# Performance work log

Measured on AMD Instinct MI355X. Metric: run time of the kernel, lower is better.

Reference implementation:

```python
import jax, jax.numpy as jnp
import numpy as np

H = 32          # hidden_size
NUM_LAYERS = 3
B, T, IN = 16384, 64, 2


def _gru_dir(x, Wih, Whh, bih, bhh, reverse):
    """Single-direction GRU over x:[B,T,I] with PyTorch gate math."""
    # Precompute input projections for all timesteps: [B,T,3H]
    xg = jnp.einsum('bti,gi->btg', x, Wih) + bih
    if reverse:
        xg = xg[:, ::-1]

    def step(h, xt):
        gh = h @ Whh.T + bhh                      # [B,3H]
        xr, xz, xn = jnp.split(xt, 3, axis=-1)
        hr, hz, hn = jnp.split(gh, 3, axis=-1)
        r = jax.nn.sigmoid(xr + hr)
        z = jax.nn.sigmoid(xz + hz)
        n = jnp.tanh(xn + r * hn)
        h2 = (1.0 - z) * n + z * h
        return h2, h2

    h0 = jnp.zeros((x.shape[0], H), x.dtype)
    _, hs = jax.lax.scan(step, h0, jnp.swapaxes(xg, 0, 1))  # [T,B,H]
    hs = jnp.swapaxes(hs, 0, 1)                              # [B,T,H]
    if reverse:
        hs = hs[:, ::-1]
    return hs


def setup_inputs() -> dict:
    key = jax.random.key(0)
    ks = jax.random.split(key, 11)
    s = 0.2  # weight scale ~ uniform(-1/sqrt(H)) magnitude
    return {
        'x':    jax.random.normal(ks[0], (B, T, IN), jnp.float32),
        'Wih0': jax.random.normal(ks[1], (2, 3 * H, IN), jnp.float32) * s,
        'Whh0': jax.random.normal(ks[2], (2, 3 * H, H), jnp.float32) * s,
        'bih0': jax.random.normal(ks[3], (2, 3 * H), jnp.float32) * s,
        'bhh0': jax.random.normal(ks[4], (2, 3 * H), jnp.float32) * s,
        'Wih':  jax.random.normal(ks[5], (NUM_LAYERS - 1, 2, 3 * H, 2 * H), jnp.float32) * s,
        'Whh':  jax.random.normal(ks[6], (NUM_LAYERS - 1, 2, 3 * H, H), jnp.float32) * s,
        'bih':  jax.random.normal(ks[7], (NUM_LAYERS - 1, 2, 3 * H), jnp.float32) * s,
        'bhh':  jax.random.normal(ks[8], (NUM_LAYERS - 1, 2, 3 * H), jnp.float32) * s,
        'Wfc':  jax.random.normal(ks[9], (2, 2 * H), jnp.float32) * s,
        'bfc':  jax.random.normal(ks[10], (2,), jnp.float32) * s,
    }


def reference(x, Wih0, Whh0, bih0, bhh0, Wih, Whh, bih, bhh, Wfc, bfc):
    out = x
    for l in range(NUM_LAYERS):
        if l == 0:
            wi, wh, bi, bh = Wih0, Whh0, bih0, bhh0
        else:
            wi, wh, bi, bh = Wih[l - 1], Whh[l - 1], bih[l - 1], bhh[l - 1]
        fwd = _gru_dir(out, wi[0], wh[0], bi[0], bh[0], reverse=False)
        bwd = _gru_dir(out, wi[1], wh[1], bi[1], bh[1], reverse=True)
        out = jnp.concatenate([fwd, bwd], axis=-1)  # [B,T,2H]
    y = out @ Wfc.T + bfc                            # [B,T,2]
    return jnp.tanh(y)
```

## Files before the change

kernel.cpp:

```cpp
#include <hip/hip_runtime.h>
#include <cstdint>
#include <cstddef>


#define BB 16384
#define TT 64
#define PS ((size_t)BB * 32)
#define DS ((size_t)TT * PS)
#define PT ((size_t)TT * BB * 2)

typedef __attribute__((ext_vector_type(8))) _Float16 f16x8;
typedef __attribute__((ext_vector_type(4))) float f32x4;
typedef __attribute__((ext_vector_type(2))) float f32x2;

#if __has_builtin(__builtin_amdgcn_exp2f)
#define EXP2(x) __builtin_amdgcn_exp2f(x)
#else
#define EXP2(x) exp2f(x)
#endif
#if __has_builtin(__builtin_amdgcn_rcpf)
#define RCP(x) __builtin_amdgcn_rcpf(x)
#else
#define RCP(x) (1.0f / (x))
#endif

#define SR (-1.4426950408889634f)
#define SN (-2.8853900817779268f)

__device__ __forceinline__ f32x2 mk2(float a, float b) {
    f32x2 v; v.x = a; v.y = b; return v;
}
__device__ __forceinline__ float tanh_fast(float x) { return 2.0f / (1.0f + __expf(-2.0f * x)) - 1.0f; }
__device__ __forceinline__ unsigned short f2h(float f) {
    _Float16 h = (_Float16)f;
    return __builtin_bit_cast(unsigned short, h);
}
__device__ __forceinline__ unsigned int cvt_pkh(float a, float b) {
#if __has_builtin(__builtin_amdgcn_cvt_pkrtz)
    typedef __fp16 h2_t __attribute__((ext_vector_type(2)));
    h2_t p = __builtin_amdgcn_cvt_pkrtz(a, b);
    return __builtin_bit_cast(unsigned int, p);
#else
    return (unsigned int)f2h(a) | ((unsigned int)f2h(b) << 16);
#endif
}
__device__ __forceinline__ f32x4 mfma16h(f16x8 a, f16x8 b, f32x4 c) {
    return __builtin_amdgcn_mfma_f32_16x16x32_f16(a, b, c, 0, 0, 0);
}

__device__ __forceinline__ void gate_pair2(f32x2 aR, f32x2 aZ, f32x2 xN, f32x2 hN,
                                           f32x2& hp) {
    f32x2 er = mk2(EXP2(aR.x), EXP2(aR.y));
    f32x2 ez = mk2(EXP2(aZ.x), EXP2(aZ.y));
    f32x2 Ar = er + 1.f;
    f32x2 Az = ez + 1.f;
    float iR = RCP(Ar.x * Ar.y);
    float iZ = RCP(Az.x * Az.y);
    f32x2 r = mk2(iR * Ar.y, iR * Ar.x);
    f32x2 z = mk2(iZ * Az.y, iZ * Az.x);
    f32x2 v = r * hN + xN;
    f32x2 en = mk2(EXP2(v.x), EXP2(v.y));
    f32x2 An = en + 1.f;
    float iN = RCP(An.x * An.y);
    f32x2 n = mk2(fmaf(2.f, iN * An.y, -1.f), fmaf(2.f, iN * An.x, -1.f));
    hp = z * (hp - n) + n;
}


template<bool IS_L0, bool IS_LAST>
__global__ __launch_bounds__(256, 2)
void gru_mfma(const float* __restrict__ x0,
              const unsigned short* __restrict__ bin,
              const float* __restrict__ Wih,
              const float* __restrict__ Whh,
              const float* __restrict__ bih,
              const float* __restrict__ bhh,
              unsigned short* __restrict__ bout,
              const float* __restrict__ Wfc,
              float* __restrict__ pbase)
{
    const int tid  = threadIdx.x;
    const int lane = tid & 63;
    const int wv   = tid >> 6;
    const int g    = blockIdx.x * 4 + wv;
    const int d    = g >> 10;
    const int b0   = (g & 1023) * 16;
    const int col  = lane & 15;
    const int qd   = lane >> 4;

    f16x8 whhF[6];
    {
        const float* wsrc = Whh + d * 96 * 32;
        #pragma unroll
        for (int t = 0; t < 6; ++t) {
            const float sc = (t < 4) ? SR : SN;
            const int row = (t >> 1) * 32 + 8 * (col >> 2) + 4 * (t & 1) + (col & 3);
            const float* pr = wsrc + row * 32 + qd * 8;
            unsigned short wbits[8];
            #pragma unroll
            for (int j = 0; j < 8; ++j) wbits[j] = f2h(pr[j] * sc);
            whhF[t] = __builtin_bit_cast(f16x8, *(uint4*)wbits);
        }
    }

    f16x8 wihF[6][2];
    float w0c[6][4], w1c[6][4];
    if constexpr (!IS_L0) {
        const float* wsrc = Wih + d * 96 * 64;
        #pragma unroll
        for (int t = 0; t < 6; ++t) {
            const float sc = (t < 4) ? SR : SN;
            const int row = (t >> 1) * 32 + 8 * (col >> 2) + 4 * (t & 1) + (col & 3);
            #pragma unroll
            for (int kc = 0; kc < 2; ++kc) {
                const float* pr = wsrc + row * 64 + kc * 32 + qd * 8;
                unsigned short wbits[8];
                #pragma unroll
                for (int j = 0; j < 8; ++j) wbits[j] = f2h(pr[j] * sc);
                wihF[t][kc] = __builtin_bit_cast(f16x8, *(uint4*)wbits);
            }
        }
    } else {
        #pragma unroll
        for (int t = 0; t < 6; ++t) {
            const float sc = (t < 4) ? SR : SN;
            #pragma unroll
            for (int q = 0; q < 4; ++q) {
                const int row = (t >> 1) * 32 + 8 * qd + 4 * (t & 1) + q;
                const float* pr = Wih + d * 96 * 2 + row * 2;
                w0c[t][q] = pr[0] * sc;
                w1c[t][q] = pr[1] * sc;
            }
        }
    }

    f32x4 biasIn[6], biasHN[2];
    {
        const float* bi = bih + d * 96;
        const float* bh = bhh + d * 96;
        #pragma unroll
        for (int t = 0; t < 4; ++t) {
            const int off = (t >> 1) * 32 + 8 * qd + 4 * (t & 1);
            float4 a = *(const float4*)(bi + off);
            float4 b = *(const float4*)(bh + off);
            biasIn[t][0] = (a.x + b.x) * SR; biasIn[t][1] = (a.y + b.y) * SR;
            biasIn[t][2] = (a.z + b.z) * SR; biasIn[t][3] = (a.w + b.w) * SR;
        }
        #pragma unroll
        for (int T = 0; T < 2; ++T) {
            const int off = 64 + 8 * qd + 4 * T;
            float4 a = *(const float4*)(bi + off);
            float4 b = *(const float4*)(bh + off);
            biasIn[4 + T][0] = a.x * SN; biasIn[4 + T][1] = a.y * SN;
            biasIn[4 + T][2] = a.z * SN; biasIn[4 + T][3] = a.w * SN;
            biasHN[T][0] = b.x * SN; biasHN[T][1] = b.y * SN;
            biasHN[T][2] = b.z * SN; biasHN[T][3] = b.w * SN;
        }
    }

    float wf0[2][4], wf1[2][4];
    if constexpr (IS_LAST) {
        #pragma unroll
        for (int T = 0; T < 2; ++T)
            #pragma unroll
            for (int q = 0; q < 4; ++q) {
                const int u = 8 * qd + 4 * T + q;
                wf0[T][q] = Wfc[d * 32 + u];
                wf1[T][q] = Wfc[64 + d * 32 + u];
            }
    }

    const int t0 = d ? (TT - 1) : 0;
    const int dt = d ? -1 : 1;
    const ptrdiff_t dplane = (ptrdiff_t)dt * (ptrdiff_t)PS;

    f16x8 hF = {};
    float hprev[2][4] = {{0.f,0.f,0.f,0.f},{0.f,0.f,0.f,0.f}};

    auto REC = [&](f32x4 (&acc)[6], f32x4 (&accHN)[2]) {
        #pragma unroll
        for (int t = 0; t < 4; ++t)
            acc[t] = mfma16h(whhF[t], hF, acc[t]);
        #pragma unroll
        for (int T = 0; T < 2; ++T)
            accHN[T] = mfma16h(whhF[4 + T], hF, biasHN[T]);
    };

    auto PROJ = [&](f32x4 (&accN)[6], uint4 nx0, uint4 nx1, float2 nxs) {
        if constexpr (!IS_L0) {
            f16x8 a0 = __builtin_bit_cast(f16x8, nx0);
            f16x8 a1 = __builtin_bit_cast(f16x8, nx1);
            #pragma unroll
            for (int t = 0; t < 6; ++t) {
                accN[t] = mfma16h(wihF[t][0], a0, biasIn[t]);
                accN[t] = mfma16h(wihF[t][1], a1, accN[t]);
            }
        } else {
            #pragma unroll
            for (int t = 0; t < 6; ++t)
                #pragma unroll
                for (int q = 0; q < 4; ++q)
                    accN[t][q] = fmaf(nxs.x, w0c[t][q], fmaf(nxs.y, w1c[t][q], biasIn[t][q]));
        }
    };

    auto GATES = [&](f32x4 (&acc)[6], f32x4 (&accHN)[2], unsigned short* outp,
                     uint4& hwP, unsigned short*& opP, float* poutp) {
        unsigned int hw[4];
        #pragma unroll
        for (int T = 0; T < 2; ++T) {
            f32x2 hp01 = mk2(hprev[T][0], hprev[T][1]);
            f32x2 hp23 = mk2(hprev[T][2], hprev[T][3]);
            gate_pair2(mk2(acc[T][0], acc[T][1]), mk2(acc[2 + T][0], acc[2 + T][1]),
                       mk2(acc[4 + T][0], acc[4 + T][1]), mk2(accHN[T][0], accHN[T][1]), hp01);
            gate_pair2(mk2(acc[T][2], acc[T][3]), mk2(acc[2 + T][2], acc[2 + T][3]),
                       mk2(acc[4 + T][2], acc[4 + T][3]), mk2(accHN[T][2], accHN[T][3]), hp23);
            hprev[T][0] = hp01.x; hprev[T][1] = hp01.y;
            hprev[T][2] = hp23.x; hprev[T][3] = hp23.y;
            hw[2 * T]     = cvt_pkh(hp01.x, hp01.y);
            hw[2 * T + 1] = cvt_pkh(hp23.x, hp23.y);
        }
        hF = __builtin_bit_cast(f16x8, *(uint4*)hw);
        if constexpr (IS_LAST) {
            float p0 = 0.f, p1 = 0.f;
            #pragma unroll
            for (int T = 0; T < 2; ++T)
                #pragma unroll
                for (int q = 0; q < 4; ++q) {
                    p0 = fmaf(hprev[T][q], wf0[T][q], p0);
                    p1 = fmaf(hprev[T][q], wf1[T][q], p1);
                }
            p0 += __shfl_xor(p0, 16); p0 += __shfl_xor(p0, 32);
            p1 += __shfl_xor(p1, 16); p1 += __shfl_xor(p1, 32);
            if (qd == 0) *(float2*)poutp = make_float2(p0, p1);
        } else {
            *(uint4*)opP = hwP;
            hwP = *(uint4*)hw;
            opP = outp;
        }
    };

    f32x4 accA[6], accB[6], accHN[2];
    uint4 xc0 = {}, xc1 = {}, xe0 = {}, xe1 = {};
    float2 xsc = {}, xse = {};
    const unsigned short* xFE = nullptr; const unsigned short* xBE = nullptr;
    const unsigned short* xFO = nullptr; const unsigned short* xBO = nullptr;
    const float* xfpE = nullptr; const float* xfpO = nullptr;

    if constexpr (!IS_L0) {
        const unsigned short* pF = bin + (size_t)t0 * PS + (size_t)(b0 + col) * 32 + qd * 8;
        const unsigned short* pB = pF + DS;
        uint4 a = *(const uint4*)pF, b = *(const uint4*)pB;
        PROJ(accA, a, b, {});
        xc0 = *(const uint4*)(pF + dplane);
        xc1 = *(const uint4*)(pB + dplane);
        xFE = pF + 2 * dplane; xBE = pB + 2 * dplane;
        xFO = pF + 3 * dplane; xBO = pB + 3 * dplane;
    } else {
        const float* p0 = x0 + ((size_t)(b0 + col) * TT + t0) * 2;
        float2 xs0 = *(const float2*)p0;
        PROJ(accA, {}, {}, xs0);
        xsc = *(const float2*)(p0 + dt * 2);
        xfpE = p0 + dt * 4;
        xfpO = p0 + dt * 6;
    }

    unsigned short* optrA = nullptr; unsigned short* optrB = nullptr;
    float* poutA = nullptr; float* poutB = nullptr;
    const ptrdiff_t dpp = (ptrdiff_t)dt * (ptrdiff_t)BB * 2;
    if constexpr (IS_LAST) {
        poutA = pbase + (size_t)d * PT + ((size_t)t0 * BB + b0 + col) * 2;
        poutB = poutA + dpp;
    } else {
        optrA = bout + (size_t)d * DS + (size_t)t0 * PS + (size_t)(b0 + col) * 32 + qd * 8;
        optrB = optrA + dplane;
    }

    uint4 hwPrevA = {}, hwPrevB = {};
    unsigned short* opPrevA = optrA;
    unsigned short* opPrevB = optrB;

    for (int k = 0; k < 31; ++k) {
        if constexpr (!IS_L0) {
            xe0 = *(const uint4*)xFE; xe1 = *(const uint4*)xBE;
            xFE += 2 * dplane; xBE += 2 * dplane;
        } else { xse = *(const float2*)xfpE; xfpE += dt * 4; }
        REC(accA, accHN);
        PROJ(accB, xc0, xc1, xsc);
        GATES(accA, accHN, optrA, hwPrevA, opPrevA, poutA);
        if constexpr (IS_LAST) poutA += 2 * dpp; else optrA += 2 * dplane;
        if constexpr (!IS_L0) {
            xc0 = *(const uint4*)xFO; xc1 = *(const uint4*)xBO;
            xFO += 2 * dplane; xBO += 2 * dplane;
        } else { xsc = *(const float2*)xfpO; xfpO += dt * 4; }
        REC(accB, accHN);
        PROJ(accA, xe0, xe1, xse);
        GATES(accB, accHN, optrB, hwPrevB, opPrevB, poutB);
        if constexpr (IS_LAST) poutB += 2 * dpp; else optrB += 2 * dplane;
    }
    REC(accA, accHN);
    PROJ(accB, xc0, xc1, xsc);
    GATES(accA, accHN, optrA, hwPrevA, opPrevA, poutA);
    REC(accB, accHN);
    GATES(accB, accHN, optrB, hwPrevB, opPrevB, poutB);
    if constexpr (!IS_LAST) {
        *(uint4*)opPrevA = hwPrevA;
        *(uint4*)opPrevB = hwPrevB;
    }
}

__global__ __launch_bounds__(256)
void fc_finish(const float* __restrict__ pf,
               const float* __restrict__ pb,
               const float* __restrict__ bfc,
               float* __restrict__ out)
{
    __shared__ float2 tile[64][65];
    const int tid = threadIdx.x;
    const int bbase = blockIdx.x * 64;
    const float c0 = bfc[0], c1 = bfc[1];
    #pragma unroll
    for (int tp = 0; tp < 16; ++tp) {
        const int t = tp * 4 + (tid >> 6);
        const int bl = tid & 63;
        const size_t idx = ((size_t)t * BB + bbase + bl) * 2;
        float2 vf = *(const float2*)(pf + idx);
        float2 vb = *(const float2*)(pb + idx);
        float2 o;
        o.x = tanh_fast(vf.x + vb.x + c0);
        o.y = tanh_fast(vf.y + vb.y + c1);
        tile[t][bl] = o;
    }
    __syncthreads();
    #pragma unroll
    for (int bp = 0; bp < 16; ++bp) {
        const int bl = bp * 4 + (tid >> 6);
        const int t = tid & 63;
        *(float2*)(out + ((size_t)(bbase + bl) * TT + t) * 2) = tile[t][bl];
    }
}

extern "C" void kernel_launch(void* const* d_in, const int* in_sizes, int n_in,
                              void* d_out, int out_size, void* d_ws, size_t ws_size,
                              hipStream_t stream)
{
    const float* x    = (const float*)d_in[0];
    const float* Wih0 = (const float*)d_in[1];
    const float* Whh0 = (const float*)d_in[2];
    const float* bih0 = (const float*)d_in[3];
    const float* bhh0 = (const float*)d_in[4];
    const float* WihL = (const float*)d_in[5];
    const float* WhhL = (const float*)d_in[6];
    const float* bihL = (const float*)d_in[7];
    const float* bhhL = (const float*)d_in[8];
    const float* Wfc  = (const float*)d_in[9];
    const float* bfc  = (const float*)d_in[10];

    unsigned short* buf0 = (unsigned short*)d_ws;
    unsigned short* buf1 = buf0 + 2 * DS;
    float* pbase = (float*)d_ws;
    float* out = (float*)d_out;

    gru_mfma<true, false><<<512, 256, 0, stream>>>(
        x, nullptr, Wih0, Whh0, bih0, bhh0, buf0, nullptr, nullptr);
    gru_mfma<false, false><<<512, 256, 0, stream>>>(
        nullptr, buf0, WihL, WhhL, bihL, bhhL, buf1, nullptr, nullptr);
    gru_mfma<false, true><<<512, 256, 0, stream>>>(
        nullptr, buf1, WihL + 2 * 96 * 64, WhhL + 2 * 96 * 32,
        bihL + 2 * 96, bhhL + 2 * 96, nullptr, Wfc, pbase);
    fc_finish<<<BB / 64, 256, 0, stream>>>(
        pbase, pbase + PT, bfc, out);
}
```

Before: 267.7 us.

## Fuse all GRU layers and FC finish into one cooperative persistent kernel

Replaces the four separate launches (three GRU layers plus the FC/tanh finish) with one cooperative kernel of 256 blocks of 512 threads that runs each layer body in turn, separated by grid-wide syncs. This removes per-launch overhead and the gaps between kernels. In exchange it changes the block shape (8 waves per block) and adds the cost of grid barriers. If the cooperative launch fails, it falls back to the original multi-kernel path.

Result: slower. 563.1 us (+110.3%).

```diff
diff --git a/kernel.cpp b/kernel.cpp
--- a/kernel.cpp
+++ b/kernel.cpp
@@ -1,7 +1,10 @@
 #include <hip/hip_runtime.h>
+#include <hip/hip_cooperative_groups.h>
 #include <cstdint>
 #include <cstddef>
 
+
+namespace cg = cooperative_groups;
 
 #define BB 16384
 #define TT 64
@@ -68,8 +71,9 @@
 
 
 template<bool IS_L0, bool IS_LAST>
-__global__ __launch_bounds__(256, 2)
-void gru_mfma(const float* __restrict__ x0,
+__device__ __forceinline__ void gru_layer_body(
+              int g,
+              const float* __restrict__ x0,
               const unsigned short* __restrict__ bin,
               const float* __restrict__ Wih,
               const float* __restrict__ Whh,
@@ -81,8 +85,6 @@
 {
     const int tid  = threadIdx.x;
     const int lane = tid & 63;
-    const int wv   = tid >> 6;
-    const int g    = blockIdx.x * 4 + wv;
     const int d    = g >> 10;
     const int b0   = (g & 1023) * 16;
     const int col  = lane & 15;
@@ -309,19 +311,13 @@
     }
 }
 
-__global__ __launch_bounds__(256)
-void fc_finish(const float* __restrict__ pf,
-               const float* __restrict__ pb,
-               const float* __restrict__ bfc,
-               float* __restrict__ out)
-{
-    __shared__ float2 tile[64][65];
+__device__ __forceinline__ void fc_fin_body(const float* pf, const float* pb,
+                                            float c0, float c1, float* out,
+                                            int bbase, float2 (*tile)[65])
+{
     const int tid = threadIdx.x;
-    const int bbase = blockIdx.x * 64;
-    const float c0 = bfc[0], c1 = bfc[1];
-    #pragma unroll
-    for (int tp = 0; tp < 16; ++tp) {
-        const int t = tp * 4 + (tid >> 6);
+    const int nt = blockDim.x >> 6;
+    for (int t = tid >> 6; t < 64; t += nt) {
         const int bl = tid & 63;
         const size_t idx = ((size_t)t * BB + bbase + bl) * 2;
         float2 vf = *(const float2*)(pf + idx);
@@ -332,12 +328,60 @@
         tile[t][bl] = o;
     }
     __syncthreads();
-    #pragma unroll
-    for (int bp = 0; bp < 16; ++bp) {
-        const int bl = bp * 4 + (tid >> 6);
+    for (int bl = tid >> 6; bl < 64; bl += nt) {
         const int t = tid & 63;
         *(float2*)(out + ((size_t)(bbase + bl) * TT + t) * 2) = tile[t][bl];
     }
+}
+
+template<bool IS_L0, bool IS_LAST>
+__global__ __launch_bounds__(256, 2)
+void gru_mfma(const float* __restrict__ x0, const unsigned short* __restrict__ bin,
+              const float* __restrict__ Wih, const float* __restrict__ Whh,
+              const float* __restrict__ bih, const float* __restrict__ bhh,
+              unsigned short* __restrict__ bout,
+              const float* __restrict__ Wfc, float* __restrict__ pbase)
+{
+    const int g = blockIdx.x * 4 + (threadIdx.x >> 6);
+    gru_layer_body<IS_L0, IS_LAST>(g, x0, bin, Wih, Whh, bih, bhh, bout, Wfc, pbase);
+}
+
+__global__ __launch_bounds__(256)
+void fc_finish(const float* __restrict__ pf, const float* __restrict__ pb,
+               const float* __restrict__ bfc, float* __restrict__ out)
+{
+    __shared__ float2 tile[64][65];
+    fc_fin_body(pf, pb, bfc[0], bfc[1], out, blockIdx.x * 64, tile);
+}
+
+__global__ __launch_bounds__(512, 2)
+void gru_net(const float* x,
+             const float* Wih0, const float* Whh0,
+             const float* bih0, const float* bhh0,
+             const float* WihL, const float* WhhL,
+             const float* bihL, const float* bhhL,
+             const float* Wfc,  const float* bfc,
+             unsigned short* buf0, unsigned short* buf1,
+             float* pbase, float* out)
+{
+    __shared__ float2 tile[64][65];
+    cg::grid_group grid = cg::this_grid();
+    const int g = blockIdx.x * 8 + (threadIdx.x >> 6);
+
+    gru_layer_body<true, false>(g, x, nullptr, Wih0, Whh0, bih0, bhh0,
+                                buf0, nullptr, nullptr);
+    __threadfence();
+    grid.sync();
+    gru_layer_body<false, false>(g, nullptr, buf0, WihL, WhhL, bihL, bhhL,
+                                 buf1, nullptr, nullptr);
+    __threadfence();
+    grid.sync();
+    gru_layer_body<false, true>(g, nullptr, buf1, WihL + 2 * 96 * 64, WhhL + 2 * 96 * 32,
+                                bihL + 2 * 96, bhhL + 2 * 96, nullptr, Wfc, pbase);
+    __threadfence();
+    grid.sync();
+
+    fc_fin_body(pbase, pbase + PT, bfc[0], bfc[1], out, blockIdx.x * 64, tile);
 }
 
 extern "C" void kernel_launch(void* const* d_in, const int* in_sizes, int n_in,
@@ -361,13 +405,24 @@
     float* pbase = (float*)d_ws;
     float* out = (float*)d_out;
 
-    gru_mfma<true, false><<<512, 256, 0, stream>>>(
-        x, nullptr, Wih0, Whh0, bih0, bhh0, buf0, nullptr, nullptr);
-    gru_mfma<false, false><<<512, 256, 0, stream>>>(
-        nullptr, buf0, WihL, WhhL, bihL, bhhL, buf1, nullptr, nullptr);
-    gru_mfma<false, true><<<512, 256, 0, stream>>>(
-        nullptr, buf1, WihL + 2 * 96 * 64, WhhL + 2 * 96 * 32,
-        bihL + 2 * 96, bhhL + 2 * 96, nullptr, Wfc, pbase);
-    fc_finish<<<BB / 64, 256, 0, stream>>>(
-        pbase, pbase + PT, bfc, out);
-}
+    void* args[] = {
+        (void*)&x, (void*)&Wih0, (void*)&Whh0, (void*)&bih0, (void*)&bhh0,
+        (void*)&WihL, (void*)&WhhL, (void*)&bihL, (void*)&bhhL,
+        (void*)&Wfc, (void*)&bfc,
+        (void*)&buf0, (void*)&buf1, (void*)&pbase, (void*)&out
+    };
+    hipError_t err = hipLaunchCooperativeKernel((void*)gru_net, dim3(256), dim3(512),
+                                                args, 0, stream);
+    if (err != hipSuccess) {
+        (void)hipGetLastError();
+        gru_mfma<true, false><<<512, 256, 0, stream>>>(
+            x, nullptr, Wih0, Whh0, bih0, bhh0, buf0, nullptr, nullptr);
+        gru_mfma<false, false><<<512, 256, 0, stream>>>(
+            nullptr, buf0, WihL, WhhL, bihL, bhhL, buf1, nullptr, nullptr);
+        gru_mfma<false, true><<<512, 256, 0, stream>>>(
+            nullptr, buf1, WihL + 2 * 96 * 64, WhhL + 2 * 96 * 32,
+            bihL + 2 * 96, bhhL + 2 * 96, nullptr, Wfc, pbase);
+        fc_finish<<<BB / 64, 256, 0, stream>>>(
+            pbase, pbase + PT, bfc, out);
+    }
+}
```
